# Performance work log

Measured on AMD Instinct MI355X. Metric: run time of the kernel, lower is better.

Reference implementation:

```python
import jax, jax.numpy as jnp
import numpy as np

B, L, D_IN, D_MODEL, D_OUT, N_LAYERS, N2 = 16, 2048, 512, 512, 512, 4, 32
Q_STEP = 1.0 / 64.0
LN_EPS = 1e-5


def setup_inputs() -> dict:
    key = jax.random.key(0)
    ks = jax.random.split(key, 12)
    H = D_MODEL
    x = jax.random.normal(ks[0], (B, D_IN, L), jnp.float32)
    # sigma-delta dense encoder / decoder weights (ANN-equivalent: dense + ReLU)
    W_enc = jax.random.normal(ks[1], (H, D_IN), jnp.float32) * (1.0 / np.sqrt(D_IN))
    W_dec = jax.random.normal(ks[2], (D_OUT, H), jnp.float32) * (1.0 / np.sqrt(H))
    # S4D kernel params, stacked over layers. S4D-Lin init.
    log_dt = (jax.random.uniform(ks[3], (N_LAYERS, H), jnp.float32)
              * (np.log(0.1) - np.log(0.001)) + np.log(0.001))
    log_A_real = jnp.full((N_LAYERS, H, N2), np.log(0.5), jnp.float32)
    A_imag = jnp.tile((np.pi * jnp.arange(N2, dtype=jnp.float32))[None, None, :],
                      (N_LAYERS, H, 1))
    C_re = jax.random.normal(ks[4], (N_LAYERS, H, N2), jnp.float32) * (0.5 ** 0.5)
    C_im = jax.random.normal(ks[5], (N_LAYERS, H, N2), jnp.float32) * (0.5 ** 0.5)
    D = jax.random.normal(ks[6], (N_LAYERS, H), jnp.float32)
    # output linear of each S4D block: 1x1 conv H -> 2H followed by GLU
    W_out = jax.random.normal(ks[7], (N_LAYERS, 2 * H, H), jnp.float32) * (1.0 / np.sqrt(H))
    b_out = jnp.zeros((N_LAYERS, 2 * H), jnp.float32)
    ln_g = jnp.ones((N_LAYERS, H), jnp.float32)
    ln_b = jnp.zeros((N_LAYERS, H), jnp.float32)
    return {"x": x, "W_enc": W_enc, "W_dec": W_dec, "log_dt": log_dt,
            "log_A_real": log_A_real, "A_imag": A_imag, "C_re": C_re,
            "C_im": C_im, "D": D, "W_out": W_out, "b_out": b_out,
            "ln_g": ln_g, "ln_b": ln_b}


def _quantize_ste(x, step):
    q = jnp.round(x / step) * step
    return x + jax.lax.stop_gradient(q - x)


def reference(x, W_enc, W_dec, log_dt, log_A_real, A_imag, C_re, C_im, D,
              W_out, b_out, ln_g, ln_b):
    # x: (B, d_input, L) channel-time layout (slayer convention)
    xq = _quantize_ste(x, Q_STEP)
    h = jax.nn.relu(jnp.einsum('bct,dc->bdt', xq, W_enc))  # encoder (B,H,L)
    Lx = h.shape[-1]
    t = jnp.arange(Lx)
    for i in range(N_LAYERS):
        # ---- S4D kernel (ZOH-style discretization) ----
        dt = jnp.exp(log_dt[i])[:, None]                 # (H,1)
        A = -jnp.exp(log_A_real[i]) + 1j * A_imag[i]     # (H,N)
        dtA = dt * A                                     # (H,N)
        Cc = (C_re[i] + 1j * C_im[i]) * jnp.expm1(dtA) / A
        vand = jnp.exp(dtA[:, :, None] * t)              # (H,N,L)
        K = 2.0 * jnp.einsum('hn,hnl->hl', Cc, vand).real  # (H,L)
        # ---- FFT convolution ----
        k_f = jnp.fft.rfft(K, n=2 * Lx)                  # (H, L+1)
        u_f = jnp.fft.rfft(h, n=2 * Lx)                  # (B,H,L+1)
        y = jnp.fft.irfft(u_f * k_f[None], n=2 * Lx)[..., :Lx]
        y = y + D[i][:, None] * h                        # skip connection
        y = jax.nn.gelu(y, approximate=False)
        # output linear: 1x1 conv H->2H + GLU over channel dim
        z = jnp.einsum('bht,dh->bdt', y, W_out[i]) + b_out[i][None, :, None]
        z = z[:, :D_MODEL] * jax.nn.sigmoid(z[:, D_MODEL:])
        # residual + post-norm (LayerNorm over channel dim)
        h = z + h
        mu = h.mean(axis=1, keepdims=True)
        var = h.var(axis=1, keepdims=True)
        h = (h - mu) / jnp.sqrt(var + LN_EPS) * ln_g[i][:, None] + ln_b[i][:, None]
    out = jax.nn.relu(jnp.einsum('bht,dh->bdt', h, W_dec))  # decoder (B,d_out,L)
    return out
```

## Files before the change

### kernel.cpp

```cpp
#include <hip/hip_runtime.h>
#include <cstdint>
#include <cstddef>

typedef __attribute__((ext_vector_type(8))) short short8;
typedef __attribute__((ext_vector_type(8))) _Float16 half8;
typedef __attribute__((ext_vector_type(4))) float floatx4;
typedef __attribute__((ext_vector_type(4))) int intx4;
typedef __attribute__((ext_vector_type(4))) unsigned short ushort4v;

__device__ __forceinline__ unsigned short f2h(float f) {
    union { _Float16 h; unsigned short u; } v;
    v.h = (_Float16)f;
    return v.u;
}
__device__ __forceinline__ float relu_keepnan(float v) {
    return v > 0.f ? v : (v == v ? 0.f : v);
}

__global__ __launch_bounds__(256) void k_cvt(
    const float* __restrict__ src, unsigned short* __restrict__ dst, int n) {
    int i = blockIdx.x * 256 + threadIdx.x;
    if (i < n) dst[i] = f2h(src[i]);
}

__global__ __launch_bounds__(256) void k_precompute(
    const float* __restrict__ ldt, const float* __restrict__ lar,
    const float* __restrict__ aim, const float* __restrict__ cre,
    const float* __restrict__ cim, float4* __restrict__ lwc,
    float2* __restrict__ wt) {
    int idx = blockIdx.x * 256 + threadIdx.x;
    int i = idx >> 14;
    int h = (idx >> 5) & 511;
    int n = idx & 31;
    float dt = expf(ldt[i * 512 + h]);
    float Are = -expf(lar[idx]);
    float Aim = aim[idx];
    float dre = dt * Are, dim = dt * Aim;
    float e = expf(dre);
    float wre = e * cosf(dim);
    float wim = e * sinf(dim);
    float emr = wre - 1.f, emi = wim;
    float inv = 1.f / (Are * Are + Aim * Aim);
    float fr = (emr * Are + emi * Aim) * inv;
    float fi = (emi * Are - emr * Aim) * inv;
    float cr = cre[idx], ci = cim[idx];
    float4 o;
    o.x = wre; o.y = wim;
    o.z = 2.f * (cr * fr - ci * fi);
    o.w = 2.f * (cr * fi + ci * fr);
    int oidx = (i * 32 + n) * 512 + h;
    lwc[oidx] = o;
    float ar = wre, ai = wim;
#pragma unroll
    for (int k = 0; k < 7; ++k) {
        float nr = ar * ar - ai * ai;
        float ni = 2.f * ar * ai;
        ar = nr; ai = ni;
    }
    wt[oidx] = make_float2(ar, ai);
}

__global__ __launch_bounds__(256) void k_quant_transpose(
    const float* __restrict__ x, unsigned short* __restrict__ xq, int b0) {
    __shared__ unsigned short tile[64][65];
    const int bg = b0 + blockIdx.z, bl = blockIdx.z;
    const int c0 = blockIdx.y * 64, t0 = blockIdx.x * 64;
    const int tid = threadIdx.x;
#pragma unroll
    for (int it = 0; it < 16; ++it) {
        int idx = it * 256 + tid;
        int r = idx >> 6, cc = idx & 63;
        float f = x[(size_t)(bg * 512 + c0 + r) * 2048 + t0 + cc];
        float q = rintf(f * 64.f) * 0.015625f;
        tile[r][cc] = f2h(q);
    }
    __syncthreads();
#pragma unroll
    for (int it = 0; it < 16; ++it) {
        int idx = it * 256 + tid;
        int r = idx >> 6, cc = idx & 63;
        xq[(size_t)(bl * 2048 + t0 + r) * 512 + c0 + cc] = tile[cc][r];
    }
}

__global__ __launch_bounds__(64) void k_build_wa(
    const float4* __restrict__ lwc, unsigned short* __restrict__ WA, int layer) {
    __shared__ unsigned short Ws[64 * 136];
    const int h = blockIdx.x, tid = threadIdx.x;
    if (tid < 32) {
        float4 v = lwc[((size_t)layer * 32 + tid) * 512 + h];
        float pr = 1.f, pi = 0.f;
        for (int m = 0; m < 128; ++m) {
            Ws[(2 * tid) * 136 + (127 - m)] = f2h(pr);
            Ws[(2 * tid + 1) * 136 + (127 - m)] = f2h(pi);
            float nr = pr * v.x - pi * v.y;
            float ni = pr * v.y + pi * v.x;
            pr = nr; pi = ni;
        }
    }
    __syncthreads();
#pragma unroll
    for (int it = 0; it < 16; ++it) {
        int idx = it * 64 + tid;
        int r = idx >> 4, c8 = idx & 15;
        *(intx4*)(WA + (size_t)h * 8192 + r * 128 + c8 * 8) =
            *(const intx4*)(Ws + r * 136 + c8 * 8);
    }
}

__global__ __launch_bounds__(256) void k_build_T(
    const float4* __restrict__ lwc, const float* __restrict__ Dp,
    unsigned short* __restrict__ TT, int layer) {
    __shared__ float Kvs[128];
    __shared__ unsigned short Mxs[128 * 64];
    __shared__ float wr_s[32], wi_s[32], cr_s[32], ci_s[32];
    const int h = blockIdx.x, tid = threadIdx.x;
    if (tid < 32) {
        float4 v = lwc[((size_t)layer * 32 + tid) * 512 + h];
        wr_s[tid] = v.x; wi_s[tid] = v.y; cr_s[tid] = v.z; ci_s[tid] = v.w;
    }
    __syncthreads();
    if (tid < 32) {
        const int n = tid;
        float wre = wr_s[n], wim = wi_s[n];
        float ar = cr_s[n], ai = ci_s[n];
        for (int m = 0; m <= 128; ++m) {
            if (m < 128) {
                float s = ar;
#pragma unroll
                for (int d = 16; d >= 1; d >>= 1) s += __shfl_xor(s, d, 64);
                if (n == 0) Kvs[m] = s;
            }
            if (m >= 1) {
                Mxs[(m - 1) * 64 + 2 * n] = f2h(ar);
                Mxs[(m - 1) * 64 + 2 * n + 1] = f2h(-ai);
            }
            float nr = ar * wre - ai * wim;
            float ni = ar * wim + ai * wre;
            ar = nr; ai = ni;
        }
    }
    __syncthreads();
    const float Dh = Dp[layer * 512 + h];
#pragma unroll
    for (int it = 0; it < 12; ++it) {
        int idx = it * 256 + tid;
        int t = idx / 24, c8 = idx % 24;
        short8 pack;
#pragma unroll
        for (int q = 0; q < 8; ++q) {
            int k = c8 * 8 + q;
            unsigned short us;
            if (k < 128) {
                float val = (k <= t) ? (Kvs[t - k] + (k == t ? Dh : 0.f)) : 0.f;
                us = f2h(val);
            } else {
                us = Mxs[t * 64 + (k - 128)];
            }
            pack[q] = (short)us;
        }
        *(short8*)(TT + (size_t)h * 24576 + t * 192 + c8 * 8) = pack;
    }
}

template <int MODE>
__global__ __launch_bounds__(256, 2) void k_gemm(
    const unsigned short* __restrict__ A, const unsigned short* __restrict__ Bm,
    float* __restrict__ of32, unsigned short* __restrict__ ut, int J, int b0) {
    __shared__ __align__(16) unsigned short lds[2 * 128 * 72];
    unsigned short* Al = lds;
    unsigned short* Bl = lds + 128 * 72;
    const int tid = threadIdx.x;
    const int m0 = blockIdx.y * 128;
    const int j0 = blockIdx.x * 128;
    const int sub = tid & 7;
    const int row = tid >> 3;
    const unsigned short* Ag = A + (size_t)(m0 + row) * 512 + sub * 8;
    const unsigned short* Bg = Bm + (size_t)(j0 + row) * 512 + sub * 8;
    intx4 ra[4], rb[4];
#pragma unroll
    for (int i = 0; i < 4; ++i) {
        ra[i] = *(const intx4*)(Ag + (size_t)i * 32 * 512);
        rb[i] = *(const intx4*)(Bg + (size_t)i * 32 * 512);
    }
    const int lane = tid & 63;
    const int w = tid >> 6;
    const int wm = w & 1, wn = w >> 1;
    const int l15 = lane & 15, quad = lane >> 4;
    floatx4 acc[4][4] = {};
    for (int kt = 0; kt < 8; ++kt) {
#pragma unroll
        for (int i = 0; i < 4; ++i) {
            *(intx4*)(Al + (row + 32 * i) * 72 + sub * 8) = ra[i];
            *(intx4*)(Bl + (row + 32 * i) * 72 + sub * 8) = rb[i];
        }
        __syncthreads();
        if (kt < 7) {
#pragma unroll
            for (int i = 0; i < 4; ++i) {
                ra[i] = *(const intx4*)(Ag + (size_t)i * 32 * 512 + (kt + 1) * 64);
                rb[i] = *(const intx4*)(Bg + (size_t)i * 32 * 512 + (kt + 1) * 64);
            }
        }
#pragma unroll
        for (int ks = 0; ks < 2; ++ks) {
            half8 af[4], bfr[4];
#pragma unroll
            for (int mt = 0; mt < 4; ++mt)
                af[mt] = *(const half8*)(Al + (wm * 64 + mt * 16 + l15) * 72 + ks * 32 + quad * 8);
#pragma unroll
            for (int nt = 0; nt < 4; ++nt)
                bfr[nt] = *(const half8*)(Bl + (wn * 64 + nt * 16 + l15) * 72 + ks * 32 + quad * 8);
#pragma unroll
            for (int mt = 0; mt < 4; ++mt)
#pragma unroll
                for (int nt = 0; nt < 4; ++nt)
                    acc[mt][nt] = __builtin_amdgcn_mfma_f32_16x16x32_f16(
                        af[mt], bfr[nt], acc[mt][nt], 0, 0, 0);
        }
        __syncthreads();
    }
#pragma unroll
    for (int mt = 0; mt < 4; ++mt) {
#pragma unroll
        for (int nt = 0; nt < 4; ++nt) {
            const int dl = wm * 64 + mt * 16 + quad * 4;
            const int jl = wn * 64 + nt * 16 + l15;
            floatx4 v = acc[mt][nt];
#pragma unroll
            for (int r = 0; r < 4; ++r) v[r] = relu_keepnan(v[r]);
            if (MODE == 0) {
                *(floatx4*)(of32 + (size_t)(j0 + jl) * 512 + m0 + dl) = v;
#pragma unroll
                for (int r = 0; r < 4; ++r) lds[(dl + r) * 136 + jl] = f2h(v[r]);
            } else {
                const int j = j0 + jl;
                const int bl = j >> 11, t = j & 2047;
#pragma unroll
                for (int r = 0; r < 4; ++r)
                    of32[((size_t)((b0 + bl) * 512 + m0 + dl + r)) * 2048 + t] = v[r];
            }
        }
    }
    if (MODE == 0) {
        __syncthreads();
        const int drow = tid >> 1, hh = tid & 1;
        const unsigned short* srcp = lds + drow * 136 + hh * 64;
        unsigned short* dstp = ut + (size_t)(m0 + drow) * J + j0 + hh * 64;
#pragma unroll
        for (int q = 0; q < 8; ++q)
            *(intx4*)(dstp + q * 8) = *(const intx4*)(srcp + q * 8);
    }
}

__global__ __launch_bounds__(256, 4) void k_stateA(
    const unsigned short* __restrict__ WA, const unsigned short* __restrict__ ut,
    float* __restrict__ P, int J, int Rtot) {
    __shared__ __align__(16) unsigned short Aw[64 * 72];
    __shared__ __align__(16) unsigned short Bw[128 * 72];
    const int tid = threadIdx.x;
    const int h = blockIdx.y;
    const int r0 = blockIdx.x * 128;
    const int sub = tid & 7, row = tid >> 3;
    const unsigned short* Ag = WA + (size_t)h * 8192 + row * 128 + sub * 8;
    const unsigned short* Bg = ut + (size_t)h * J + (size_t)(r0 + row) * 128 + sub * 8;
    intx4 ra[2], rb[4];
    ra[0] = *(const intx4*)(Ag);
    ra[1] = *(const intx4*)(Ag + 32 * 128);
#pragma unroll
    for (int i = 0; i < 4; ++i) rb[i] = *(const intx4*)(Bg + i * 32 * 128);
    const int lane = tid & 63, w = tid >> 6;
    const int wm = w & 1, wn = w >> 1;
    const int l15 = lane & 15, quad = lane >> 4;
    floatx4 acc[2][4] = {};
    for (int kt = 0; kt < 2; ++kt) {
        *(intx4*)(Aw + row * 72 + sub * 8) = ra[0];
        *(intx4*)(Aw + (row + 32) * 72 + sub * 8) = ra[1];
#pragma unroll
        for (int i = 0; i < 4; ++i)
            *(intx4*)(Bw + (row + 32 * i) * 72 + sub * 8) = rb[i];
        __syncthreads();
        if (kt == 0) {
            ra[0] = *(const intx4*)(Ag + 64);
            ra[1] = *(const intx4*)(Ag + 32 * 128 + 64);
#pragma unroll
            for (int i = 0; i < 4; ++i) rb[i] = *(const intx4*)(Bg + i * 32 * 128 + 64);
        }
#pragma unroll
        for (int ks = 0; ks < 2; ++ks) {
            half8 af[2], bfr[4];
#pragma unroll
            for (int mt = 0; mt < 2; ++mt)
                af[mt] = *(const half8*)(Aw + (wm * 32 + mt * 16 + l15) * 72 + ks * 32 + quad * 8);
#pragma unroll
            for (int nt = 0; nt < 4; ++nt)
                bfr[nt] = *(const half8*)(Bw + (wn * 64 + nt * 16 + l15) * 72 + ks * 32 + quad * 8);
#pragma unroll
            for (int mt = 0; mt < 2; ++mt)
#pragma unroll
                for (int nt = 0; nt < 4; ++nt)
                    acc[mt][nt] = __builtin_amdgcn_mfma_f32_16x16x32_f16(
                        af[mt], bfr[nt], acc[mt][nt], 0, 0, 0);
        }
        __syncthreads();
    }
#pragma unroll
    for (int mt = 0; mt < 2; ++mt)
#pragma unroll
        for (int nt = 0; nt < 4; ++nt)
#pragma unroll
            for (int r = 0; r < 4; ++r)
                P[((size_t)h * 64 + wm * 32 + mt * 16 + quad * 4 + r) * Rtot +
                  r0 + wn * 64 + nt * 16 + l15] = acc[mt][nt][r];
}

__global__ __launch_bounds__(64) void k_comb(
    const float* __restrict__ P, const float2* __restrict__ wt,
    unsigned short* __restrict__ S0, int layer, int Rtot) {
    __shared__ float Ps[64][17];
    __shared__ unsigned short S0s[16][64];
    const int h = blockIdx.x, bl = blockIdx.y;
    const int tid = threadIdx.x;
#pragma unroll
    for (int it = 0; it < 4; ++it) {
        int idx = it * 64 + tid;
        int n2 = idx >> 2, pt = idx & 3;
        float4 v = *(const float4*)(P + ((size_t)h * 64 + n2) * Rtot + bl * 16 + pt * 4);
        Ps[n2][pt * 4 + 0] = v.x; Ps[n2][pt * 4 + 1] = v.y;
        Ps[n2][pt * 4 + 2] = v.z; Ps[n2][pt * 4 + 3] = v.w;
    }
    __syncthreads();
    if (tid < 32) {
        const int n = tid;
        float2 wv = wt[((size_t)layer * 32 + n) * 512 + h];
        float ar = 0.f, ai = 0.f;
        for (int g = 0; g < 16; ++g) {
            S0s[g][2 * n] = f2h(ar);
            S0s[g][2 * n + 1] = f2h(ai);
            float pr = Ps[2 * n][g], pi = Ps[2 * n + 1][g];
            float nr = fmaf(wv.x, ar, fmaf(-wv.y, ai, pr));
            float ni = fmaf(wv.x, ai, fmaf(wv.y, ar, pi));
            ar = nr; ai = ni;
        }
    }
    __syncthreads();
    const int g = tid >> 2, pt = tid & 3;
    unsigned short* dst = S0 + ((size_t)h * Rtot + bl * 16 + g) * 64 + pt * 16;
    *(intx4*)(dst) = *(const intx4*)(&S0s[g][pt * 16]);
    *(intx4*)(dst + 8) = *(const intx4*)(&S0s[g][pt * 16 + 8]);
}

__global__ __launch_bounds__(256, 2) void k_applyB(
    const unsigned short* __restrict__ TT, const unsigned short* __restrict__ ut,
    const unsigned short* __restrict__ S0, unsigned short* __restrict__ vt,
    int J, int Rtot) {
    __shared__ __align__(16) unsigned short lds[2 * 128 * 72];
    unsigned short* Al = lds;
    unsigned short* Bl = lds + 128 * 72;
    const int tid = threadIdx.x;
    const int h = blockIdx.y;
    const int r0 = blockIdx.x * 128;
    const int sub = tid & 7, row = tid >> 3;
    const unsigned short* Ag = TT + (size_t)h * 24576 + row * 192 + sub * 8;
    const unsigned short* Bu = ut + (size_t)h * J + (size_t)(r0 + row) * 128 + sub * 8;
    const unsigned short* Bs = S0 + ((size_t)h * Rtot + r0 + row) * 64 + sub * 8;
    intx4 ra[4], rb[4];
#pragma unroll
    for (int i = 0; i < 4; ++i) {
        ra[i] = *(const intx4*)(Ag + i * 32 * 192);
        rb[i] = *(const intx4*)(Bu + i * 32 * 128);
    }
    const int lane = tid & 63, w = tid >> 6;
    const int wm = w & 1, wn = w >> 1;
    const int l15 = lane & 15, quad = lane >> 4;
    floatx4 acc[4][4] = {};
    for (int kt = 0; kt < 3; ++kt) {
#pragma unroll
        for (int i = 0; i < 4; ++i) {
            *(intx4*)(Al + (row + 32 * i) * 72 + sub * 8) = ra[i];
            *(intx4*)(Bl + (row + 32 * i) * 72 + sub * 8) = rb[i];
        }
        __syncthreads();
        if (kt == 0) {
#pragma unroll
            for (int i = 0; i < 4; ++i) {
                ra[i] = *(const intx4*)(Ag + i * 32 * 192 + 64);
                rb[i] = *(const intx4*)(Bu + i * 32 * 128 + 64);
            }
        } else if (kt == 1) {
#pragma unroll
            for (int i = 0; i < 4; ++i) {
                ra[i] = *(const intx4*)(Ag + i * 32 * 192 + 128);
                rb[i] = *(const intx4*)(Bs + i * 32 * 64);
            }
        }
#pragma unroll
        for (int ks = 0; ks < 2; ++ks) {
            half8 af[4], bfr[4];
#pragma unroll
            for (int mt = 0; mt < 4; ++mt)
                af[mt] = *(const half8*)(Al + (wm * 64 + mt * 16 + l15) * 72 + ks * 32 + quad * 8);
#pragma unroll
            for (int nt = 0; nt < 4; ++nt)
                bfr[nt] = *(const half8*)(Bl + (wn * 64 + nt * 16 + l15) * 72 + ks * 32 + quad * 8);
#pragma unroll
            for (int mt = 0; mt < 4; ++mt)
#pragma unroll
                for (int nt = 0; nt < 4; ++nt)
                    acc[mt][nt] = __builtin_amdgcn_mfma_f32_16x16x32_f16(
                        af[mt], bfr[nt], acc[mt][nt], 0, 0, 0);
        }
        __syncthreads();
    }
#pragma unroll
    for (int mt = 0; mt < 4; ++mt)
#pragma unroll
        for (int nt = 0; nt < 4; ++nt) {
            const int tl = wm * 64 + mt * 16 + quad * 4;
            const int rl = wn * 64 + nt * 16 + l15;
            ushort4v pack;
#pragma unroll
            for (int r = 0; r < 4; ++r) {
                float y = acc[mt][nt][r];
                float ge = 0.5f * y * (1.f + erff(y * 0.70710678118654752f));
                pack[r] = f2h(ge);
            }
            *(ushort4v*)(lds + rl * 136 + tl) = pack;
        }
    __syncthreads();
    const int rl2 = tid >> 1, hh = tid & 1;
    const unsigned short* srcp = lds + rl2 * 136 + hh * 64;
    unsigned short* dstp = vt + (size_t)h * J + (size_t)(r0 + rl2) * 128 + hh * 64;
#pragma unroll
    for (int q = 0; q < 8; ++q)
        *(intx4*)(dstp + q * 8) = *(const intx4*)(srcp + q * 8);
}

__global__ __launch_bounds__(256, 2) void k_gemm_glu(
    const unsigned short* __restrict__ A,
    const unsigned short* __restrict__ Bt,
    const float* __restrict__ bias,
    float* __restrict__ g_out, int J) {
    __shared__ __align__(16) unsigned short A1l[128 * 72];
    __shared__ __align__(16) unsigned short A2l[128 * 72];
    __shared__ __align__(16) unsigned short Bl[128 * 72];
    const int tid = threadIdx.x;
    const int m0 = blockIdx.y * 128;
    const int j0 = blockIdx.x * 128;
    const int sub = tid & 7;
    const int row = tid >> 3;
    const unsigned short* A1g = A + (size_t)(m0 + row) * 512 + sub * 8;
    const unsigned short* A2g = A1g + 512 * 512;
    const int chp = tid >> 3, jo = tid & 7;
    const unsigned short* Bg = Bt + (size_t)(2 * chp) * J + j0 + jo * 8;
    intx4 ra1[4], ra2[4], rb[4];
#pragma unroll
    for (int i = 0; i < 4; ++i) {
        ra1[i] = *(const intx4*)(A1g + (size_t)i * 32 * 512);
        ra2[i] = *(const intx4*)(A2g + (size_t)i * 32 * 512);
    }
    rb[0] = *(const intx4*)(Bg);
    rb[1] = *(const intx4*)(Bg + J);
    rb[2] = *(const intx4*)(Bg + 64);
    rb[3] = *(const intx4*)(Bg + J + 64);
    const int lane = tid & 63;
    const int w = tid >> 6;
    const int wm = w & 1, wn = w >> 1;
    const int l15 = lane & 15, quad = lane >> 4;
    const int colbase = (((chp >> 2) ^ jo) << 3) + (chp & 3) * 2;
    floatx4 ac1[4][4] = {}, ac2[4][4] = {};
    for (int kt = 0; kt < 8; ++kt) {
#pragma unroll
        for (int i = 0; i < 4; ++i) {
            *(intx4*)(A1l + (row + 32 * i) * 72 + sub * 8) = ra1[i];
            *(intx4*)(A2l + (row + 32 * i) * 72 + sub * 8) = ra2[i];
        }
        {
            unsigned int* B32 = (unsigned int*)Bl;
#pragma unroll
            for (int half = 0; half < 2; ++half) {
                const int jb = (jo + half * 8) * 8;
                intx4 e0 = rb[half * 2], e1 = rb[half * 2 + 1];
#pragma unroll
                for (int i = 0; i < 4; ++i) {
                    unsigned int ae = (unsigned int)e0[i], be = (unsigned int)e1[i];
                    unsigned int lo = (ae & 0xffffu) | (be << 16);
                    unsigned int hi = (ae >> 16) | (be & 0xffff0000u);
                    B32[((jb + 2 * i) * 72 + colbase) >> 1] = lo;
                    B32[((jb + 2 * i + 1) * 72 + colbase) >> 1] = hi;
                }
            }
        }
        __syncthreads();
        if (kt < 7) {
#pragma unroll
            for (int i = 0; i < 4; ++i) {
                ra1[i] = *(const intx4*)(A1g + (size_t)i * 32 * 512 + (kt + 1) * 64);
                ra2[i] = *(const intx4*)(A2g + (size_t)i * 32 * 512 + (kt + 1) * 64);
            }
            rb[0] = *(const intx4*)(Bg + (size_t)(kt + 1) * 64 * J);
            rb[1] = *(const intx4*)(Bg + (size_t)(kt + 1) * 64 * J + J);
            rb[2] = *(const intx4*)(Bg + (size_t)(kt + 1) * 64 * J + 64);
            rb[3] = *(const intx4*)(Bg + (size_t)(kt + 1) * 64 * J + J + 64);
        }
#pragma unroll
        for (int ks = 0; ks < 2; ++ks) {
            half8 af1[4], af2[4], bfr[4];
#pragma unroll
            for (int mt = 0; mt < 4; ++mt) {
                af1[mt] = *(const half8*)(A1l + (wm * 64 + mt * 16 + l15) * 72 + ks * 32 + quad * 8);
                af2[mt] = *(const half8*)(A2l + (wm * 64 + mt * 16 + l15) * 72 + ks * 32 + quad * 8);
            }
#pragma unroll
            for (int nt = 0; nt < 4; ++nt) {
                const int rr = wn * 64 + nt * 16 + l15;
                const int cb = (ks * 4 + quad) ^ ((rr >> 3) & 7);
                bfr[nt] = *(const half8*)(Bl + rr * 72 + cb * 8);
            }
#pragma unroll
            for (int mt = 0; mt < 4; ++mt)
#pragma unroll
                for (int nt = 0; nt < 4; ++nt) {
                    ac1[mt][nt] = __builtin_amdgcn_mfma_f32_16x16x32_f16(
                        af1[mt], bfr[nt], ac1[mt][nt], 0, 0, 0);
                    ac2[mt][nt] = __builtin_amdgcn_mfma_f32_16x16x32_f16(
                        af2[mt], bfr[nt], ac2[mt][nt], 0, 0, 0);
                }
        }
        __syncthreads();
    }
#pragma unroll
    for (int mt = 0; mt < 4; ++mt) {
#pragma unroll
        for (int nt = 0; nt < 4; ++nt) {
            const int d = m0 + wm * 64 + mt * 16 + quad * 4;
            const int j = j0 + wn * 64 + nt * 16 + l15;
            floatx4 v;
#pragma unroll
            for (int r = 0; r < 4; ++r) {
                float a = ac1[mt][nt][r] + bias[d + r];
                float gg = ac2[mt][nt][r] + bias[512 + d + r];
                v[r] = a / (1.f + expf(-gg));
            }
            *(floatx4*)(g_out + (size_t)j * 512 + d) = v;
        }
    }
}

__global__ __launch_bounds__(256, 4) void k_res_ln_t(
    const float* __restrict__ g, float* __restrict__ hf,
    unsigned short* __restrict__ ut, unsigned short* __restrict__ hb,
    const float* __restrict__ lng, const float* __restrict__ lnb,
    int layer, int J, int mode) {
    __shared__ unsigned short tile[64 * 40];
    const int tid = threadIdx.x;
    const int r = tid >> 3, sub = tid & 7;
    const int j0 = blockIdx.x * 32;
    const size_t j = (size_t)j0 + r;
    const float* gj = g + j * 512;
    float* hj = hf + j * 512;
    floatx4 v[16];
    float s1 = 0.f, s2 = 0.f;
#pragma unroll
    for (int k = 0; k < 16; ++k) {
        floatx4 gv = *(const floatx4*)(gj + sub * 4 + k * 32);
        floatx4 hv = *(const floatx4*)(hj + sub * 4 + k * 32);
        floatx4 vv = gv + hv;
        v[k] = vv;
        s1 += vv[0] + vv[1] + vv[2] + vv[3];
        s2 += vv[0] * vv[0] + vv[1] * vv[1] + vv[2] * vv[2] + vv[3] * vv[3];
    }
#pragma unroll
    for (int m = 4; m >= 1; m >>= 1) { s1 += __shfl_xor(s1, m, 64); s2 += __shfl_xor(s2, m, 64); }
    const float mu = s1 * (1.f / 512.f);
    const float var = s2 * (1.f / 512.f) - mu * mu;
    const float isd = 1.f / sqrtf(var + 1e-5f);
#pragma unroll
    for (int t = 0; t < 8; ++t) {
        if (mode == 1 && t) __syncthreads();
#pragma unroll
        for (int kk = 0; kk < 2; ++kk) {
            const int k = t * 2 + kk;
            const int cho = sub * 4 + k * 32;
            floatx4 gw = *(const floatx4*)(lng + layer * 512 + cho);
            floatx4 bw = *(const floatx4*)(lnb + layer * 512 + cho);
            floatx4 o;
#pragma unroll
            for (int i = 0; i < 4; ++i) o[i] = (v[k][i] - mu) * isd * gw[i] + bw[i];
            *(floatx4*)(hj + cho) = o;
            if (mode == 1) {
                const int chl = kk * 32 + sub * 4;
#pragma unroll
                for (int i = 0; i < 4; ++i)
                    tile[(chl + i) * 40 + (r ^ ((((chl + i) >> 2) & 3) << 3))] = f2h(o[i]);
            } else {
                ushort4v p;
#pragma unroll
                for (int i = 0; i < 4; ++i) p[i] = f2h(o[i]);
                *(ushort4v*)(hb + j * 512 + cho) = p;
            }
        }
        if (mode == 1) {
            __syncthreads();
            const int chrow = tid >> 2, part = tid & 3;
            const int pb = part ^ ((chrow >> 2) & 3);
            *(intx4*)(ut + (size_t)(t * 64 + chrow) * J + j0 + part * 8) =
                *(const intx4*)(tile + chrow * 40 + pb * 8);
        }
    }
}

extern "C" void kernel_launch(void* const* d_in, const int* in_sizes, int n_in,
                              void* d_out, int out_size, void* d_ws, size_t ws_size,
                              hipStream_t stream) {
    (void)in_sizes; (void)n_in; (void)out_size;
    const float* x      = (const float*)d_in[0];
    const float* W_enc  = (const float*)d_in[1];
    const float* W_dec  = (const float*)d_in[2];
    const float* log_dt = (const float*)d_in[3];
    const float* log_Ar = (const float*)d_in[4];
    const float* A_im   = (const float*)d_in[5];
    const float* C_re   = (const float*)d_in[6];
    const float* C_im   = (const float*)d_in[7];
    const float* Dp     = (const float*)d_in[8];
    const float* W_out  = (const float*)d_in[9];
    const float* b_out  = (const float*)d_in[10];
    const float* ln_g   = (const float*)d_in[11];
    const float* ln_b   = (const float*)d_in[12];

    int C = 16;
    while (C > 8 && (size_t)C * (12ull << 20) + (41ull << 20) > ws_size) C >>= 1;
    const size_t J = (size_t)C * 2048;
    const int Rtot = C * 16;

    char* ws = (char*)d_ws;
    size_t off = 0;
    auto alloc = [&](size_t bytes) { void* p = ws + off; off += (bytes + 255) & ~(size_t)255; return p; };
    float4*         lwc   = (float4*)alloc(4ull * 512 * 32 * 16);
    float2*         wt    = (float2*)alloc(4ull * 512 * 32 * 8);
    unsigned short* wencb = (unsigned short*)alloc(512 * 512 * 2);
    unsigned short* wdecb = (unsigned short*)alloc(512 * 512 * 2);
    unsigned short* woutb = (unsigned short*)alloc(4ull * 1024 * 512 * 2);
    unsigned short* WAb   = (unsigned short*)alloc(512ull * 64 * 128 * 2);
    unsigned short* TTb   = (unsigned short*)alloc(512ull * 128 * 192 * 2);
    unsigned short* ut    = (unsigned short*)alloc(512ull * J * 2);
    float*          g     = (float*)alloc(J * 512 * 4);
    float*          hf    = (float*)alloc(J * 512 * 4);
    unsigned short* vt    = (unsigned short*)alloc(J * 512 * 2);
    unsigned short* xq    = (unsigned short*)g;
    unsigned short* hb    = vt;
    float*          P     = (float*)g;
    unsigned short* S0u   = (unsigned short*)((char*)g + (size_t)C * (2ull << 20));

    k_precompute<<<256, 256, 0, stream>>>(log_dt, log_Ar, A_im, C_re, C_im, lwc, wt);
    k_cvt<<<1024, 256, 0, stream>>>(W_enc, wencb, 512 * 512);
    k_cvt<<<1024, 256, 0, stream>>>(W_dec, wdecb, 512 * 512);
    k_cvt<<<8192, 256, 0, stream>>>(W_out, woutb, 4 * 1024 * 512);
    for (int b0 = 0; b0 < 16; b0 += C) {
        k_quant_transpose<<<dim3(32, 8, C), 256, 0, stream>>>(x, xq, b0);
        k_gemm<0><<<dim3(C * 16, 4), 256, 0, stream>>>(wencb, xq, hf, ut, (int)J, 0);
        for (int i = 0; i < 4; ++i) {
            k_build_wa<<<512, 64, 0, stream>>>(lwc, WAb, i);
            k_build_T<<<512, 256, 0, stream>>>(lwc, Dp, TTb, i);
            k_stateA<<<dim3(Rtot / 128, 512), 256, 0, stream>>>(WAb, ut, P, (int)J, Rtot);
            k_comb<<<dim3(512, C), 64, 0, stream>>>(P, wt, S0u, i, Rtot);
            k_applyB<<<dim3(Rtot / 128, 512), 256, 0, stream>>>(TTb, ut, S0u, vt, (int)J, Rtot);
            k_gemm_glu<<<dim3(C * 16, 4), 256, 0, stream>>>(
                woutb + (size_t)i * 1024 * 512, vt, b_out + (size_t)i * 1024, g, (int)J);
            k_res_ln_t<<<(int)(J / 32), 256, 0, stream>>>(
                g, hf, ut, hb, ln_g, ln_b, i, (int)J, (i == 3) ? 2 : 1);
        }
        k_gemm<2><<<dim3(C * 16, 4), 256, 0, stream>>>(wdecb, hb, (float*)d_out, nullptr, 0, b0);
    }
}
```

Measured before the change: 975.5 us.

## Store residual and GLU output in fp16 and shrink GLU GEMM K-tile

The residual stream hf and the GLU output g move from fp32 to fp16, which halves the bytes written by the encoder/GLU GEMMs and read by the residual-LayerNorm kernel. The GLU GEMM K-tile drops from 64 to 32 with a new LDS swizzle, cutting shared memory per block and raising the occupancy hint from 2 to 5. The workspace shrinks, so the batch chunk C may stay larger. In exchange, the residual path loses precision by being rounded to fp16 after every layer, and each block now runs more K iterations with more barriers.

```diff
diff --git a/kernel.cpp b/kernel.cpp
--- a/kernel.cpp
+++ b/kernel.cpp
@@ -12,6 +12,11 @@
     union { _Float16 h; unsigned short u; } v;
     v.h = (_Float16)f;
     return v.u;
+}
+__device__ __forceinline__ float h2f(unsigned short u) {
+    union { unsigned short u; _Float16 h; } v;
+    v.u = u;
+    return (float)v.h;
 }
 __device__ __forceinline__ float relu_keepnan(float v) {
     return v > 0.f ? v : (v == v ? 0.f : v);
@@ -166,7 +171,8 @@
 template <int MODE>
 __global__ __launch_bounds__(256, 2) void k_gemm(
     const unsigned short* __restrict__ A, const unsigned short* __restrict__ Bm,
-    float* __restrict__ of32, unsigned short* __restrict__ ut, int J, int b0) {
+    float* __restrict__ of32, unsigned short* __restrict__ o16,
+    unsigned short* __restrict__ ut, int J, int b0) {
     __shared__ __align__(16) unsigned short lds[2 * 128 * 72];
     unsigned short* Al = lds;
     unsigned short* Bl = lds + 128 * 72;
@@ -230,9 +236,12 @@
 #pragma unroll
             for (int r = 0; r < 4; ++r) v[r] = relu_keepnan(v[r]);
             if (MODE == 0) {
-                *(floatx4*)(of32 + (size_t)(j0 + jl) * 512 + m0 + dl) = v;
-#pragma unroll
-                for (int r = 0; r < 4; ++r) lds[(dl + r) * 136 + jl] = f2h(v[r]);
+                ushort4v hv;
+#pragma unroll
+                for (int r = 0; r < 4; ++r) hv[r] = f2h(v[r]);
+                *(ushort4v*)(o16 + (size_t)(j0 + jl) * 512 + m0 + dl) = hv;
+#pragma unroll
+                for (int r = 0; r < 4; ++r) lds[(dl + r) * 136 + jl] = hv[r];
             } else {
                 const int j = j0 + jl;
                 const int bl = j >> 11, t = j & 2047;
@@ -436,86 +445,76 @@
         *(intx4*)(dstp + q * 8) = *(const intx4*)(srcp + q * 8);
 }
 
-__global__ __launch_bounds__(256, 2) void k_gemm_glu(
+__global__ __launch_bounds__(256, 5) void k_gemm_glu(
     const unsigned short* __restrict__ A,
     const unsigned short* __restrict__ Bt,
     const float* __restrict__ bias,
-    float* __restrict__ g_out, int J) {
-    __shared__ __align__(16) unsigned short A1l[128 * 72];
-    __shared__ __align__(16) unsigned short A2l[128 * 72];
-    __shared__ __align__(16) unsigned short Bl[128 * 72];
+    unsigned short* __restrict__ g_out, int J) {
+    __shared__ __align__(16) unsigned short A1l[128 * 36];
+    __shared__ __align__(16) unsigned short A2l[128 * 36];
+    __shared__ __align__(16) unsigned short Bl[128 * 36];
     const int tid = threadIdx.x;
     const int m0 = blockIdx.y * 128;
     const int j0 = blockIdx.x * 128;
-    const int sub = tid & 7;
-    const int row = tid >> 3;
-    const unsigned short* A1g = A + (size_t)(m0 + row) * 512 + sub * 8;
+    const int arow = tid >> 1, ah = tid & 1;
+    const unsigned short* A1g = A + (size_t)(m0 + arow) * 512 + ah * 16;
     const unsigned short* A2g = A1g + 512 * 512;
-    const int chp = tid >> 3, jo = tid & 7;
+    const int chp = tid >> 4, jo = tid & 15;
     const unsigned short* Bg = Bt + (size_t)(2 * chp) * J + j0 + jo * 8;
-    intx4 ra1[4], ra2[4], rb[4];
-#pragma unroll
-    for (int i = 0; i < 4; ++i) {
-        ra1[i] = *(const intx4*)(A1g + (size_t)i * 32 * 512);
-        ra2[i] = *(const intx4*)(A2g + (size_t)i * 32 * 512);
+    intx4 ra1[2], ra2[2], rb[2];
+#pragma unroll
+    for (int c = 0; c < 2; ++c) {
+        ra1[c] = *(const intx4*)(A1g + c * 8);
+        ra2[c] = *(const intx4*)(A2g + c * 8);
     }
     rb[0] = *(const intx4*)(Bg);
     rb[1] = *(const intx4*)(Bg + J);
-    rb[2] = *(const intx4*)(Bg + 64);
-    rb[3] = *(const intx4*)(Bg + J + 64);
     const int lane = tid & 63;
     const int w = tid >> 6;
     const int wm = w & 1, wn = w >> 1;
     const int l15 = lane & 15, quad = lane >> 4;
-    const int colbase = (((chp >> 2) ^ jo) << 3) + (chp & 3) * 2;
+    const int cwr = (chp >> 2) ^ ((jo >> 1) & 3);
+    const int bpos = chp & 3;
     floatx4 ac1[4][4] = {}, ac2[4][4] = {};
-    for (int kt = 0; kt < 8; ++kt) {
-#pragma unroll
-        for (int i = 0; i < 4; ++i) {
-            *(intx4*)(A1l + (row + 32 * i) * 72 + sub * 8) = ra1[i];
-            *(intx4*)(A2l + (row + 32 * i) * 72 + sub * 8) = ra2[i];
+    for (int kt = 0; kt < 16; ++kt) {
+#pragma unroll
+        for (int c = 0; c < 2; ++c) {
+            *(intx4*)(A1l + arow * 36 + (ah * 2 + c) * 8) = ra1[c];
+            *(intx4*)(A2l + arow * 36 + (ah * 2 + c) * 8) = ra2[c];
         }
         {
             unsigned int* B32 = (unsigned int*)Bl;
 #pragma unroll
-            for (int half = 0; half < 2; ++half) {
-                const int jb = (jo + half * 8) * 8;
-                intx4 e0 = rb[half * 2], e1 = rb[half * 2 + 1];
-#pragma unroll
-                for (int i = 0; i < 4; ++i) {
-                    unsigned int ae = (unsigned int)e0[i], be = (unsigned int)e1[i];
-                    unsigned int lo = (ae & 0xffffu) | (be << 16);
-                    unsigned int hi = (ae >> 16) | (be & 0xffff0000u);
-                    B32[((jb + 2 * i) * 72 + colbase) >> 1] = lo;
-                    B32[((jb + 2 * i + 1) * 72 + colbase) >> 1] = hi;
-                }
-            }
-        }
-        __syncthreads();
-        if (kt < 7) {
-#pragma unroll
             for (int i = 0; i < 4; ++i) {
-                ra1[i] = *(const intx4*)(A1g + (size_t)i * 32 * 512 + (kt + 1) * 64);
-                ra2[i] = *(const intx4*)(A2g + (size_t)i * 32 * 512 + (kt + 1) * 64);
-            }
-            rb[0] = *(const intx4*)(Bg + (size_t)(kt + 1) * 64 * J);
-            rb[1] = *(const intx4*)(Bg + (size_t)(kt + 1) * 64 * J + J);
-            rb[2] = *(const intx4*)(Bg + (size_t)(kt + 1) * 64 * J + 64);
-            rb[3] = *(const intx4*)(Bg + (size_t)(kt + 1) * 64 * J + J + 64);
-        }
-#pragma unroll
-        for (int ks = 0; ks < 2; ++ks) {
+                unsigned int ae = (unsigned int)rb[0][i], be = (unsigned int)rb[1][i];
+                unsigned int lo = (ae & 0xffffu) | (be << 16);
+                unsigned int hi = (ae >> 16) | (be & 0xffff0000u);
+                B32[(jo * 8 + 2 * i) * 18 + cwr * 4 + bpos] = lo;
+                B32[(jo * 8 + 2 * i + 1) * 18 + cwr * 4 + bpos] = hi;
+            }
+        }
+        __syncthreads();
+        if (kt < 15) {
+#pragma unroll
+            for (int c = 0; c < 2; ++c) {
+                ra1[c] = *(const intx4*)(A1g + (kt + 1) * 32 + c * 8);
+                ra2[c] = *(const intx4*)(A2g + (kt + 1) * 32 + c * 8);
+            }
+            rb[0] = *(const intx4*)(Bg + (size_t)(kt + 1) * 32 * J);
+            rb[1] = *(const intx4*)(Bg + (size_t)(kt + 1) * 32 * J + J);
+        }
+        {
             half8 af1[4], af2[4], bfr[4];
 #pragma unroll
             for (int mt = 0; mt < 4; ++mt) {
-                af1[mt] = *(const half8*)(A1l + (wm * 64 + mt * 16 + l15) * 72 + ks * 32 + quad * 8);
-                af2[mt] = *(const half8*)(A2l + (wm * 64 + mt * 16 + l15) * 72 + ks * 32 + quad * 8);
+                af1[mt] = *(const half8*)(A1l + (wm * 64 + mt * 16 + l15) * 36 + quad * 8);
+                af2[mt] = *(const half8*)(A2l + (wm * 64 + mt * 16 + l15) * 36 + quad * 8);
             }
 #pragma unroll
             for (int nt = 0; nt < 4; ++nt) {
                 const int rr = wn * 64 + nt * 16 + l15;
-                const int cb = (ks * 4 + quad) ^ ((rr >> 3) & 7);
-                bfr[nt] = *(const half8*)(Bl + rr * 72 + cb * 8);
+                const int cb = quad ^ ((rr >> 4) & 3);
+                bfr[nt] = *(const half8*)(Bl + rr * 36 + cb * 8);
             }
 #pragma unroll
             for (int mt = 0; mt < 4; ++mt)
@@ -535,20 +534,20 @@
         for (int nt = 0; nt < 4; ++nt) {
             const int d = m0 + wm * 64 + mt * 16 + quad * 4;
             const int j = j0 + wn * 64 + nt * 16 + l15;
-            floatx4 v;
+            ushort4v v;
 #pragma unroll
             for (int r = 0; r < 4; ++r) {
                 float a = ac1[mt][nt][r] + bias[d + r];
                 float gg = ac2[mt][nt][r] + bias[512 + d + r];
-                v[r] = a / (1.f + expf(-gg));
-            }
-            *(floatx4*)(g_out + (size_t)j * 512 + d) = v;
+                v[r] = f2h(a / (1.f + expf(-gg)));
+            }
+            *(ushort4v*)(g_out + (size_t)j * 512 + d) = v;
         }
     }
 }
 
 __global__ __launch_bounds__(256, 4) void k_res_ln_t(
-    const float* __restrict__ g, float* __restrict__ hf,
+    const unsigned short* __restrict__ g, unsigned short* __restrict__ hf,
     unsigned short* __restrict__ ut, unsigned short* __restrict__ hb,
     const float* __restrict__ lng, const float* __restrict__ lnb,
     int layer, int J, int mode) {
@@ -557,15 +556,17 @@
     const int r = tid >> 3, sub = tid & 7;
     const int j0 = blockIdx.x * 32;
     const size_t j = (size_t)j0 + r;
-    const float* gj = g + j * 512;
-    float* hj = hf + j * 512;
+    const unsigned short* gj = g + j * 512;
+    unsigned short* hj = hf + j * 512;
     floatx4 v[16];
     float s1 = 0.f, s2 = 0.f;
 #pragma unroll
     for (int k = 0; k < 16; ++k) {
-        floatx4 gv = *(const floatx4*)(gj + sub * 4 + k * 32);
-        floatx4 hv = *(const floatx4*)(hj + sub * 4 + k * 32);
-        floatx4 vv = gv + hv;
+        ushort4v gv = *(const ushort4v*)(gj + sub * 4 + k * 32);
+        ushort4v hv = *(const ushort4v*)(hj + sub * 4 + k * 32);
+        floatx4 vv;
+#pragma unroll
+        for (int i = 0; i < 4; ++i) vv[i] = h2f(gv[i]) + h2f(hv[i]);
         v[k] = vv;
         s1 += vv[0] + vv[1] + vv[2] + vv[3];
         s2 += vv[0] * vv[0] + vv[1] * vv[1] + vv[2] * vv[2] + vv[3] * vv[3];
@@ -584,19 +585,17 @@
             const int cho = sub * 4 + k * 32;
             floatx4 gw = *(const floatx4*)(lng + layer * 512 + cho);
             floatx4 bw = *(const floatx4*)(lnb + layer * 512 + cho);
-            floatx4 o;
-#pragma unroll
-            for (int i = 0; i < 4; ++i) o[i] = (v[k][i] - mu) * isd * gw[i] + bw[i];
-            *(floatx4*)(hj + cho) = o;
+            ushort4v p;
+#pragma unroll
+            for (int i = 0; i < 4; ++i)
+                p[i] = f2h((v[k][i] - mu) * isd * gw[i] + bw[i]);
             if (mode == 1) {
+                *(ushort4v*)(hj + cho) = p;
                 const int chl = kk * 32 + sub * 4;
 #pragma unroll
                 for (int i = 0; i < 4; ++i)
-                    tile[(chl + i) * 40 + (r ^ ((((chl + i) >> 2) & 3) << 3))] = f2h(o[i]);
+                    tile[(chl + i) * 40 + (r ^ ((((chl + i) >> 2) & 3) << 3))] = p[i];
             } else {
-                ushort4v p;
-#pragma unroll
-                for (int i = 0; i < 4; ++i) p[i] = f2h(o[i]);
                 *(ushort4v*)(hb + j * 512 + cho) = p;
             }
         }
@@ -629,7 +628,7 @@
     const float* ln_b   = (const float*)d_in[12];
 
     int C = 16;
-    while (C > 8 && (size_t)C * (12ull << 20) + (41ull << 20) > ws_size) C >>= 1;
+    while (C > 8 && (size_t)C * (9ull << 20) + (42ull << 20) > ws_size) C >>= 1;
     const size_t J = (size_t)C * 2048;
     const int Rtot = C * 16;
 
@@ -644,13 +643,14 @@
     unsigned short* WAb   = (unsigned short*)alloc(512ull * 64 * 128 * 2);
     unsigned short* TTb   = (unsigned short*)alloc(512ull * 128 * 192 * 2);
     unsigned short* ut    = (unsigned short*)alloc(512ull * J * 2);
-    float*          g     = (float*)alloc(J * 512 * 4);
-    float*          hf    = (float*)alloc(J * 512 * 4);
+    char*           scan  = (char*)alloc((size_t)C * (3ull << 20));
+    unsigned short* hf    = (unsigned short*)alloc(J * 512 * 2);
     unsigned short* vt    = (unsigned short*)alloc(J * 512 * 2);
-    unsigned short* xq    = (unsigned short*)g;
+    unsigned short* g16   = (unsigned short*)scan;
+    unsigned short* xq    = (unsigned short*)scan;
     unsigned short* hb    = vt;
-    float*          P     = (float*)g;
-    unsigned short* S0u   = (unsigned short*)((char*)g + (size_t)C * (2ull << 20));
+    float*          P     = (float*)scan;
+    unsigned short* S0u   = (unsigned short*)(scan + (size_t)C * (2ull << 20));
 
     k_precompute<<<256, 256, 0, stream>>>(log_dt, log_Ar, A_im, C_re, C_im, lwc, wt);
     k_cvt<<<1024, 256, 0, stream>>>(W_enc, wencb, 512 * 512);
@@ -658,7 +658,7 @@
     k_cvt<<<8192, 256, 0, stream>>>(W_out, woutb, 4 * 1024 * 512);
     for (int b0 = 0; b0 < 16; b0 += C) {
         k_quant_transpose<<<dim3(32, 8, C), 256, 0, stream>>>(x, xq, b0);
-        k_gemm<0><<<dim3(C * 16, 4), 256, 0, stream>>>(wencb, xq, hf, ut, (int)J, 0);
+        k_gemm<0><<<dim3(C * 16, 4), 256, 0, stream>>>(wencb, xq, nullptr, hf, ut, (int)J, 0);
         for (int i = 0; i < 4; ++i) {
             k_build_wa<<<512, 64, 0, stream>>>(lwc, WAb, i);
             k_build_T<<<512, 256, 0, stream>>>(lwc, Dp, TTb, i);
@@ -666,10 +666,10 @@
             k_comb<<<dim3(512, C), 64, 0, stream>>>(P, wt, S0u, i, Rtot);
             k_applyB<<<dim3(Rtot / 128, 512), 256, 0, stream>>>(TTb, ut, S0u, vt, (int)J, Rtot);
             k_gemm_glu<<<dim3(C * 16, 4), 256, 0, stream>>>(
-                woutb + (size_t)i * 1024 * 512, vt, b_out + (size_t)i * 1024, g, (int)J);
+                woutb + (size_t)i * 1024 * 512, vt, b_out + (size_t)i * 1024, g16, (int)J);
             k_res_ln_t<<<(int)(J / 32), 256, 0, stream>>>(
-                g, hf, ut, hb, ln_g, ln_b, i, (int)J, (i == 3) ? 2 : 1);
-        }
-        k_gemm<2><<<dim3(C * 16, 4), 256, 0, stream>>>(wdecb, hb, (float*)d_out, nullptr, 0, b0);
-    }
-}
+                g16, hf, ut, hb, ln_g, ln_b, i, (int)J, (i == 3) ? 2 : 1);
+        }
+        k_gemm<2><<<dim3(C * 16, 4), 256, 0, stream>>>(wdecb, hb, (float*)d_out, nullptr, nullptr, (int)J, b0);
+    }
+}
```

Result: slower. 2.394 ms (+145.4%).
